# Kernel optimization log

Hardware: AMD Instinct MI355X
Metric: run time of the kernel (lower is better)

## Reference

```python
import jax, jax.numpy as jnp
import numpy as np
from jax import lax

VOCAB = 100000; E = 512; HID = 1024; H = HID // 2; T = 7; L = 4096
START = 4; STOP = 5; NEG = -10000.0


def setup_inputs() -> dict:
    key = jax.random.key(0)
    ks = jax.random.split(key, 14)
    s = 0.05  # ~1/sqrt(H), matches torch default init scale
    transitions = jax.random.normal(ks[12], (T, T), dtype=jnp.float32)
    transitions = transitions.at[START, :].set(NEG).at[:, STOP].set(NEG)
    return {
        "sentence": jax.random.randint(ks[0], (L,), 0, VOCAB),
        "emb": jax.random.normal(ks[1], (VOCAB, E), dtype=jnp.float32) * s,
        "w_ih_f": jax.random.normal(ks[2], (4 * H, E), dtype=jnp.float32) * s,
        "w_hh_f": jax.random.normal(ks[3], (4 * H, H), dtype=jnp.float32) * s,
        "b_ih_f": jax.random.normal(ks[4], (4 * H,), dtype=jnp.float32) * s,
        "b_hh_f": jax.random.normal(ks[5], (4 * H,), dtype=jnp.float32) * s,
        "w_ih_b": jax.random.normal(ks[6], (4 * H, E), dtype=jnp.float32) * s,
        "w_hh_b": jax.random.normal(ks[7], (4 * H, H), dtype=jnp.float32) * s,
        "b_ih_b": jax.random.normal(ks[8], (4 * H,), dtype=jnp.float32) * s,
        "b_hh_b": jax.random.normal(ks[9], (4 * H,), dtype=jnp.float32) * s,
        "w_out": jax.random.normal(ks[10], (T, HID), dtype=jnp.float32) * s,
        "b_out": jax.random.normal(ks[11], (T,), dtype=jnp.float32) * s,
        "transitions": transitions,
    }


def _lstm_dir(x, w_ih, w_hh, b_ih, b_hh):
    # x: [L, E] -> hidden states [L, H]; zero initial state (torch default)
    xg = x @ w_ih.T + b_ih  # [L, 4H] precomputed input gates
    h0 = jnp.zeros((H,), x.dtype)
    c0 = jnp.zeros((H,), x.dtype)
    def step(carry, g):
        h, c = carry
        gates = g + w_hh @ h + b_hh
        i, f, gg, o = jnp.split(gates, 4)
        i = jax.nn.sigmoid(i); f = jax.nn.sigmoid(f)
        gg = jnp.tanh(gg); o = jax.nn.sigmoid(o)
        c = f * c + i * gg
        h = o * jnp.tanh(c)
        return (h, c), h
    _, hs = lax.scan(step, (h0, c0), xg)
    return hs


def reference(sentence, emb, w_ih_f, w_hh_f, b_ih_f, b_hh_f,
              w_ih_b, w_hh_b, b_ih_b, b_hh_b, w_out, b_out, transitions):
    x = emb[sentence]  # [L, E]
    hf = _lstm_dir(x, w_ih_f, w_hh_f, b_ih_f, b_hh_f)            # [L, H]
    hb = _lstm_dir(x[::-1], w_ih_b, w_hh_b, b_ih_b, b_hh_b)[::-1]
    feats = jnp.concatenate([hf, hb], axis=1) @ w_out.T + b_out  # [L, T]

    # Viterbi max-plus DP
    init = jnp.full((T,), NEG, feats.dtype).at[START].set(0.0)
    def vstep(fv, feat):
        sc = fv[None, :] + transitions           # [next, prev]
        bp = jnp.argmax(sc, axis=1)
        return jnp.max(sc, axis=1) + feat, bp
    fv, bptrs = lax.scan(vstep, init, feats)     # bptrs: [L, T]
    terminal = fv + transitions[STOP]
    best = jnp.argmax(terminal)
    score = terminal[best]
    # backtrack
    def bt(tag, bp):
        return bp[tag], tag
    _, path_rev = lax.scan(bt, best, bptrs[::-1])
    best_path = path_rev[::-1]                   # [L] tag ids
    return best_path, score
```

## Files before the change

### kernel.cpp

```cpp
#include <hip/hip_runtime.h>
#include <hip/hip_bf16.h>

#define L     4096
#define E     512
#define HID   1024
#define HH    512
#define G4    2048
#define T_TAG 7
#define START_TAG 4
#define STOP_TAG  5
#define NEGV  (-10000.0f)

#define NBLK  16
#define SENT  0xFFFFFFFFu

__global__ __launch_bounds__(256)
void xg_kernel(const int* __restrict__ sentence, const float* __restrict__ emb,
               const float* __restrict__ wih_f, const float* __restrict__ bih_f,
               const float* __restrict__ bhh_f,
               const float* __restrict__ wih_b, const float* __restrict__ bih_b,
               const float* __restrict__ bhh_b,
               float* __restrict__ xg_f, float* __restrict__ xg_b)
{
    const int dir = blockIdx.z;
    const float* __restrict__ wih = dir ? wih_b : wih_f;
    const float* __restrict__ bih = dir ? bih_b : bih_f;
    const float* __restrict__ bhh = dir ? bhh_b : bhh_f;
    float* __restrict__ xg = dir ? xg_b : xg_f;

    const int t0 = blockIdx.x * 64;
    const int j0 = blockIdx.y * 64;

    __shared__ float As[32][68];
    __shared__ float Bs[32][68];
    __shared__ int   sent[64];

    const int tid = threadIdx.x;
    if (tid < 64) sent[tid] = sentence[t0 + tid];
    __syncthreads();

    const int tx = tid & 15;
    const int ty = tid >> 4;

    float acc[4][4];
#pragma unroll
    for (int a = 0; a < 4; a++)
#pragma unroll
        for (int b = 0; b < 4; b++) acc[a][b] = 0.f;

    for (int k0 = 0; k0 < E; k0 += 32) {
        __syncthreads();
#pragma unroll
        for (int q = 0; q < 2; q++) {
            const int f  = q * 256 + tid;
            const int i  = f >> 3;
            const int k4 = (f & 7) * 4;
            const float4 av = *(const float4*)(emb + (size_t)sent[i] * E + k0 + k4);
            As[k4 + 0][i] = av.x; As[k4 + 1][i] = av.y;
            As[k4 + 2][i] = av.z; As[k4 + 3][i] = av.w;
            const float4 bv = *(const float4*)(wih + (size_t)(j0 + i) * E + k0 + k4);
            Bs[k4 + 0][i] = bv.x; Bs[k4 + 1][i] = bv.y;
            Bs[k4 + 2][i] = bv.z; Bs[k4 + 3][i] = bv.w;
        }
        __syncthreads();
#pragma unroll
        for (int k = 0; k < 32; k++) {
            const float4 a4 = *(const float4*)&As[k][ty * 4];
            const float4 b4 = *(const float4*)&Bs[k][tx * 4];
            const float a[4] = { a4.x, a4.y, a4.z, a4.w };
            const float b[4] = { b4.x, b4.y, b4.z, b4.w };
#pragma unroll
            for (int ii = 0; ii < 4; ii++)
#pragma unroll
                for (int jj = 0; jj < 4; jj++) acc[ii][jj] += a[ii] * b[jj];
        }
    }

#pragma unroll
    for (int ii = 0; ii < 4; ii++) {
        const int t = t0 + ty * 4 + ii;
#pragma unroll
        for (int jj = 0; jj < 4; jj++) {
            const int j = j0 + tx * 4 + jj;
            xg[(size_t)t * G4 + j] = acc[ii][jj] + bih[j] + bhh[j];
        }
    }
}

__global__ __launch_bounds__(512)
void lstm_kernel(const float* __restrict__ xg_f, const float* __restrict__ xg_b,
                 const float* __restrict__ whh_f, const float* __restrict__ whh_b,
                 float* __restrict__ hf, float* __restrict__ hb)
{
    const int dir = blockIdx.x >> 4;
    const int rnk = blockIdx.x & 15;

    const float* __restrict__ xg  = dir ? xg_b  : xg_f;
    const float* __restrict__ whh = dir ? whh_b : whh_f;
    float* __restrict__ hout = dir ? hb : hf;

    const int tid  = threadIdx.x;
    const int wave = tid >> 6;
    const int lane = tid & 63;
    const int g    = wave >> 1;
    const int jh   = wave & 1;
    const int u0   = rnk * 32;
    const int col0 = lane * 8;

    float w[16][8];
#pragma unroll
    for (int rr = 0; rr < 16; rr++) {
        const float4* p =
            (const float4*)(whh + (size_t)(g * HH + u0 + jh * 16 + rr) * HH + col0);
        const float4 w0 = p[0], w1 = p[1];
        w[rr][0] = w0.x; w[rr][1] = w0.y; w[rr][2] = w0.z; w[rr][3] = w0.w;
        w[rr][4] = w1.x; w[rr][5] = w1.y; w[rr][6] = w1.z; w[rr][7] = w1.w;
    }

    __shared__ float h_lds[2][HH];
    __shared__ float glds[8][16];
    float c_state = 0.f;
    const int uu = u0 + (tid & 31);

    float xq0 = 0.f, xq1 = 0.f, xq2 = 0.f, xq3 = 0.f;
    if (tid < 32) {
        const float* xgt = xg + (size_t)(dir ? (L - 1) : 0) * G4;
        xq0 = xgt[uu];            xq1 = xgt[HH + uu];
        xq2 = xgt[2 * HH + uu];   xq3 = xgt[3 * HH + uu];
    }

    for (int s = 0; s < L; s++) {
        const int t = dir ? (L - 1 - s) : s;
        const int p = s & 1;

        unsigned int v = 0;
        if (s > 0) {
            const int tp = dir ? (t + 1) : (t - 1);
            const unsigned int* hp =
                (const unsigned int*)(hout + (size_t)tp * HH) + tid;
            do {
                v = __hip_atomic_load(hp, __ATOMIC_RELAXED,
                                      __HIP_MEMORY_SCOPE_AGENT);
            } while (v == SENT);
        }
        h_lds[p][tid] = __uint_as_float(v);
        __syncthreads();

        const float4 h0 = *(const float4*)&h_lds[p][col0];
        const float4 h1 = *(const float4*)&h_lds[p][col0 + 4];
        const float hv[8] = { h0.x, h0.y, h0.z, h0.w, h1.x, h1.y, h1.z, h1.w };

        float acc[16];
#pragma unroll
        for (int rr = 0; rr < 16; rr++) {
            float a = 0.f;
#pragma unroll
            for (int k = 0; k < 8; k++) a += w[rr][k] * hv[k];
            acc[rr] = a;
        }

        {
            const bool b0 = lane & 1;
#pragma unroll
            for (int r = 0; r < 8; r++) {
                const float send = b0 ? acc[r] : acc[r + 8];
                const float recv = __shfl_xor(send, 1, 64);
                acc[r] = (b0 ? acc[r + 8] : acc[r]) + recv;
            }
            const bool b1 = lane & 2;
#pragma unroll
            for (int r = 0; r < 4; r++) {
                const float send = b1 ? acc[r] : acc[r + 4];
                const float recv = __shfl_xor(send, 2, 64);
                acc[r] = (b1 ? acc[r + 4] : acc[r]) + recv;
            }
            const bool b2 = lane & 4;
#pragma unroll
            for (int r = 0; r < 2; r++) {
                const float send = b2 ? acc[r] : acc[r + 2];
                const float recv = __shfl_xor(send, 4, 64);
                acc[r] = (b2 ? acc[r + 2] : acc[r]) + recv;
            }
            const bool b3 = lane & 8;
            {
                const float send = b3 ? acc[0] : acc[1];
                const float recv = __shfl_xor(send, 8, 64);
                acc[0] = (b3 ? acc[1] : acc[0]) + recv;
            }
            acc[0] += __shfl_xor(acc[0], 16, 64);
            acc[0] += __shfl_xor(acc[0], 32, 64);
        }
        if (lane < 16) {
            const int R = ((lane & 1) << 3) | ((lane & 2) << 1) |
                          ((lane & 4) >> 1) | ((lane & 8) >> 3);
            glds[wave][R] = acc[0];
        }
        __syncthreads();

        if (tid < 32) {
            const int j   = tid;
            const int jh_ = j >> 4;
            const int rr  = j & 15;
            float iv = glds[0 + jh_][rr] + xq0;
            float fv = glds[2 + jh_][rr] + xq1;
            float gv = glds[4 + jh_][rr] + xq2;
            float ov = glds[6 + jh_][rr] + xq3;
            iv = 1.f / (1.f + expf(-iv));
            fv = 1.f / (1.f + expf(-fv));
            gv = tanhf(gv);
            ov = 1.f / (1.f + expf(-ov));
            c_state = fv * c_state + iv * gv;
            const float hval = ov * tanhf(c_state);
            __hip_atomic_store((unsigned int*)&hout[(size_t)t * HH + uu],
                               __float_as_uint(hval), __ATOMIC_RELAXED,
                               __HIP_MEMORY_SCOPE_AGENT);
            if (s + 1 < L) {
                const int tn = dir ? (t - 1) : (t + 1);
                const float* xgt = xg + (size_t)tn * G4;
                xq0 = xgt[uu];            xq1 = xgt[HH + uu];
                xq2 = xgt[2 * HH + uu];   xq3 = xgt[3 * HH + uu];
            }
        }
    }
}

__global__ __launch_bounds__(256)
void feats_kernel(const float* __restrict__ hf, const float* __restrict__ hb,
                  const float* __restrict__ wout, const float* __restrict__ bout,
                  float* __restrict__ feats)
{
    const int t   = blockIdx.x;
    const int tid = threadIdx.x;

    float acc[T_TAG];
#pragma unroll
    for (int i = 0; i < T_TAG; i++) acc[i] = 0.f;

    for (int c = tid; c < HID; c += 256) {
        const float v = (c < HH) ? hf[(size_t)t * HH + c]
                                 : hb[(size_t)t * HH + (c - HH)];
#pragma unroll
        for (int i = 0; i < T_TAG; i++) acc[i] += v * wout[i * HID + c];
    }
#pragma unroll
    for (int m = 1; m < 64; m <<= 1) {
#pragma unroll
        for (int i = 0; i < T_TAG; i++) acc[i] += __shfl_xor(acc[i], m, 64);
    }

    __shared__ float red[4][T_TAG];
    const int wave = tid >> 6, lane = tid & 63;
    if (lane == 0) {
#pragma unroll
        for (int i = 0; i < T_TAG; i++) red[wave][i] = acc[i];
    }
    __syncthreads();
    if (tid < T_TAG) {
        feats[(size_t)t * 8 + tid] =
            red[0][tid] + red[1][tid] + red[2][tid] + red[3][tid] + bout[tid];
    }
}

__global__ __launch_bounds__(64)
void viterbi_kernel(const float* __restrict__ feats, const float* __restrict__ trans,
                    float* __restrict__ out)
{
    __shared__ unsigned char bp[L][T_TAG];

    const int tid = threadIdx.x;
    const int i = tid >> 3, j = tid & 7;
    const bool valid = (i < T_TAG) && (j < T_TAG);
    const float trij = valid ? trans[i * T_TAG + j] : -1e30f;

    float fv;
    if (j < T_TAG) fv = (j == START_TAG) ? 0.f : NEGV;
    else           fv = -1e30f;

    const int ieff = (i < T_TAG) ? i : 0;
    float fq[8];
#pragma unroll
    for (int p = 0; p < 8; p++) fq[p] = feats[(size_t)p * 8 + ieff];

    for (int t = 0; t < L; t++) {
        const float sc = fv + trij;
        float best = sc; int bj = j;
#pragma unroll
        for (int m = 1; m < 8; m <<= 1) {
            const float ov = __shfl_xor(best, m, 8);
            const int   oj = __shfl_xor(bj, m, 8);
            if (ov > best || (ov == best && oj < bj)) { best = ov; bj = oj; }
        }
        const float f_t = fq[t & 7];
        if (t + 8 < L) fq[t & 7] = feats[(size_t)(t + 8) * 8 + ieff];
        const float fvnew = best + f_t;
        if (valid && j == 0) bp[t][i] = (unsigned char)bj;
        const float nf = __shfl(fvnew, (j < T_TAG) ? j * 8 : 0, 64);
        fv = (j < T_TAG) ? nf : -1e30f;
    }

    float term = fv + ((j < T_TAG) ? trans[STOP_TAG * T_TAG + j] : -1e30f);
    float bestt = term; int bt = j;
#pragma unroll
    for (int m = 1; m < 8; m <<= 1) {
        const float ov = __shfl_xor(bestt, m, 8);
        const int   oj = __shfl_xor(bt, m, 8);
        if (ov > bestt || (ov == bestt && oj < bt)) { bestt = ov; bt = oj; }
    }

    if (tid == 0) {
        out[L] = bestt;
        int tag = bt;
        out[L - 1] = (float)tag;
        for (int t = L - 1; t >= 1; t--) {
            tag = bp[t][tag];
            out[t - 1] = (float)tag;
        }
    }
}

extern "C" void kernel_launch(void* const* d_in, const int* in_sizes, int n_in,
                              void* d_out, int out_size, void* d_ws, size_t ws_size,
                              hipStream_t stream)
{
    const int*   sentence = (const int*)  d_in[0];
    const float* emb      = (const float*)d_in[1];
    const float* wih_f    = (const float*)d_in[2];
    const float* whh_f    = (const float*)d_in[3];
    const float* bih_f    = (const float*)d_in[4];
    const float* bhh_f    = (const float*)d_in[5];
    const float* wih_b    = (const float*)d_in[6];
    const float* whh_b    = (const float*)d_in[7];
    const float* bih_b    = (const float*)d_in[8];
    const float* bhh_b    = (const float*)d_in[9];
    const float* wout     = (const float*)d_in[10];
    const float* bout     = (const float*)d_in[11];
    const float* trans    = (const float*)d_in[12];
    float* out = (float*)d_out;

    char* ws = (char*)d_ws;
    float* xg_f   = (float*)(ws + 1024);
    float* xg_b   = xg_f  + (size_t)L * G4;
    float* hfbuf  = xg_b  + (size_t)L * G4;
    float* hbbuf  = hfbuf + (size_t)L * HH;
    float* featsb = hbbuf + (size_t)L * HH;

    hipMemsetAsync(hfbuf, 0xFF, (size_t)2 * L * HH * sizeof(float), stream);

    hipLaunchKernelGGL(xg_kernel, dim3(L / 64, G4 / 64, 2), dim3(256), 0, stream,
                       sentence, emb, wih_f, bih_f, bhh_f, wih_b, bih_b, bhh_b,
                       xg_f, xg_b);

    void* args[] = { (void*)&xg_f, (void*)&xg_b, (void*)&whh_f, (void*)&whh_b,
                     (void*)&hfbuf, (void*)&hbbuf };
    hipLaunchCooperativeKernel((void*)lstm_kernel, dim3(2 * NBLK), dim3(512),
                               args, 0, stream);

    hipLaunchKernelGGL(feats_kernel, dim3(L), dim3(256), 0, stream,
                       hfbuf, hbbuf, wout, bout, featsb);

    hipLaunchKernelGGL(viterbi_kernel, dim3(1), dim3(64), 0, stream,
                       featsb, trans, out);
}
```

Before: 9.976 ms.

## Assign all four gates of each unit to one wave, dropping second barrier

Reworks the recurrent weight mapping so each wave owns 4 hidden units with all four gates (16 rows), and lanes stride across columns by 64. The reduced gate sums are gathered with intra-wave shuffles, so the LDS gate buffer and the second __syncthreads per timestep go away, and 8 waves each compute 4 units in parallel instead of one group of 32 threads doing all 32. The h reads from LDS become stride-64 scalar loads instead of float4 loads, which may add LDS instructions per step.

```diff
diff --git a/kernel.cpp b/kernel.cpp
--- a/kernel.cpp
+++ b/kernel.cpp
@@ -102,31 +102,29 @@
     const int tid  = threadIdx.x;
     const int wave = tid >> 6;
     const int lane = tid & 63;
-    const int g    = wave >> 1;
-    const int jh   = wave & 1;
     const int u0   = rnk * 32;
-    const int col0 = lane * 8;
-
-    float w[16][8];
+
+    float w_reg[16][8];
 #pragma unroll
     for (int rr = 0; rr < 16; rr++) {
-        const float4* p =
-            (const float4*)(whh + (size_t)(g * HH + u0 + jh * 16 + rr) * HH + col0);
-        const float4 w0 = p[0], w1 = p[1];
-        w[rr][0] = w0.x; w[rr][1] = w0.y; w[rr][2] = w0.z; w[rr][3] = w0.w;
-        w[rr][4] = w1.x; w[rr][5] = w1.y; w[rr][6] = w1.z; w[rr][7] = w1.w;
+        const int rbit = ((rr & 1) << 3) | ((rr & 2) << 1) |
+                         ((rr & 4) >> 1) | ((rr & 8) >> 3);
+        const int gt = rbit & 3, un = rbit >> 2;
+        const size_t row = (size_t)(gt * HH + u0 + (wave << 2) + un);
+#pragma unroll
+        for (int k = 0; k < 8; k++)
+            w_reg[rr][k] = whh[row * HH + (size_t)(k * 64 + lane)];
     }
 
     __shared__ float h_lds[2][HH];
-    __shared__ float glds[8][16];
     float c_state = 0.f;
-    const int uu = u0 + (tid & 31);
-
-    float xq0 = 0.f, xq1 = 0.f, xq2 = 0.f, xq3 = 0.f;
-    if (tid < 32) {
+    const int uu = u0 + (wave << 2) + lane;
+
+    float xqi = 0.f, xqf = 0.f, xqg = 0.f, xqo = 0.f;
+    if (lane < 4) {
         const float* xgt = xg + (size_t)(dir ? (L - 1) : 0) * G4;
-        xq0 = xgt[uu];            xq1 = xgt[HH + uu];
-        xq2 = xgt[2 * HH + uu];   xq3 = xgt[3 * HH + uu];
+        xqi = xgt[uu];            xqf = xgt[HH + uu];
+        xqg = xgt[2 * HH + uu];   xqo = xgt[3 * HH + uu];
     }
 
     for (int s = 0; s < L; s++) {
@@ -146,16 +144,16 @@
         h_lds[p][tid] = __uint_as_float(v);
         __syncthreads();
 
-        const float4 h0 = *(const float4*)&h_lds[p][col0];
-        const float4 h1 = *(const float4*)&h_lds[p][col0 + 4];
-        const float hv[8] = { h0.x, h0.y, h0.z, h0.w, h1.x, h1.y, h1.z, h1.w };
+        float hv[8];
+#pragma unroll
+        for (int k = 0; k < 8; k++) hv[k] = h_lds[p][k * 64 + lane];
 
         float acc[16];
 #pragma unroll
         for (int rr = 0; rr < 16; rr++) {
             float a = 0.f;
 #pragma unroll
-            for (int k = 0; k < 8; k++) a += w[rr][k] * hv[k];
+            for (int k = 0; k < 8; k++) a += w_reg[rr][k] * hv[k];
             acc[rr] = a;
         }
 
@@ -190,21 +188,18 @@
             acc[0] += __shfl_xor(acc[0], 16, 64);
             acc[0] += __shfl_xor(acc[0], 32, 64);
         }
-        if (lane < 16) {
-            const int R = ((lane & 1) << 3) | ((lane & 2) << 1) |
-                          ((lane & 4) >> 1) | ((lane & 8) >> 3);
-            glds[wave][R] = acc[0];
-        }
-        __syncthreads();
-
-        if (tid < 32) {
-            const int j   = tid;
-            const int jh_ = j >> 4;
-            const int rr  = j & 15;
-            float iv = glds[0 + jh_][rr] + xq0;
-            float fv = glds[2 + jh_][rr] + xq1;
-            float gv = glds[4 + jh_][rr] + xq2;
-            float ov = glds[6 + jh_][rr] + xq3;
+        const float S = acc[0];
+        const int base = (lane & 3) << 2;
+        const float sv_i = __shfl(S, base + 0, 64);
+        const float sv_f = __shfl(S, base + 1, 64);
+        const float sv_g = __shfl(S, base + 2, 64);
+        const float sv_o = __shfl(S, base + 3, 64);
+
+        if (lane < 4) {
+            float iv = sv_i + xqi;
+            float fv = sv_f + xqf;
+            float gv = sv_g + xqg;
+            float ov = sv_o + xqo;
             iv = 1.f / (1.f + expf(-iv));
             fv = 1.f / (1.f + expf(-fv));
             gv = tanhf(gv);
@@ -217,8 +212,8 @@
             if (s + 1 < L) {
                 const int tn = dir ? (t - 1) : (t + 1);
                 const float* xgt = xg + (size_t)tn * G4;
-                xq0 = xgt[uu];            xq1 = xgt[HH + uu];
-                xq2 = xgt[2 * HH + uu];   xq3 = xgt[3 * HH + uu];
+                xqi = xgt[uu];            xqf = xgt[HH + uu];
+                xqg = xgt[2 * HH + uu];   xqo = xgt[3 * HH + uu];
             }
         }
     }
```

New measurement: 12.32 ms. 23.5% more time.
